# Kernel optimization log

Hardware: AMD Instinct MI355X
Metric: run time of the kernel (lower is better)

## Reference

```python
import jax, jax.numpy as jnp
import numpy as np

D_MODEL = 512
HIDDEN = 2 * D_MODEL
B, L = 8, 2048
R_MIN, R_MAX = 0.8, 0.99
LN_EPS = 1e-5


def setup_inputs() -> dict:
    key = jax.random.key(0)
    ks = jax.random.split(key, 12)
    x = jax.random.normal(ks[0], (B, L, D_MODEL), jnp.float32)
    mask = jnp.ones((B, L), jnp.float32)
    # LRU eigenvalue init, exactly as the torch __init__
    u1 = jax.random.uniform(ks[1], (HIDDEN,), jnp.float32)
    u2 = jax.random.uniform(ks[2], (HIDDEN,), jnp.float32)
    nu_log = jnp.log(-0.5 * jnp.log(u1 * (R_MAX ** 2 - R_MIN ** 2) + R_MIN ** 2))
    theta_log = jnp.log(u2 * 2.0 * np.pi)
    diag_lambda = jnp.exp(jax.lax.complex(-jnp.exp(nu_log), jnp.exp(theta_log)))
    gamma_log = jnp.log(jnp.sqrt(1.0 - jnp.abs(diag_lambda) ** 2))
    params_log = jnp.stack([nu_log, theta_log, gamma_log])  # (3, HIDDEN)
    s_in = 1.0 / np.sqrt(D_MODEL)
    s_out = 1.0 / np.sqrt(HIDDEN)
    # complex Linear weights (real+imag parts; trained weights are fully complex)
    W_in_re = jax.random.uniform(ks[3], (HIDDEN, D_MODEL), jnp.float32, -s_in, s_in)
    W_in_im = jax.random.uniform(ks[4], (HIDDEN, D_MODEL), jnp.float32, -s_in, s_in)
    b_in_re = jax.random.uniform(ks[5], (HIDDEN,), jnp.float32, -s_in, s_in)
    b_in_im = jax.random.uniform(ks[6], (HIDDEN,), jnp.float32, -s_in, s_in)
    W_out_re = jax.random.uniform(ks[7], (D_MODEL, HIDDEN), jnp.float32, -s_out, s_out)
    W_out_im = jax.random.uniform(ks[8], (D_MODEL, HIDDEN), jnp.float32, -s_out, s_out)
    b_out_re = jax.random.uniform(ks[9], (D_MODEL,), jnp.float32, -s_out, s_out)
    b_out_im = jax.random.uniform(ks[10], (D_MODEL,), jnp.float32, -s_out, s_out)
    ln_w = jnp.ones((D_MODEL,), jnp.float32)
    ln_b = jnp.zeros((D_MODEL,), jnp.float32)
    return dict(x=x, mask=mask, params_log=params_log,
                W_in_re=W_in_re, W_in_im=W_in_im, b_in_re=b_in_re, b_in_im=b_in_im,
                W_out_re=W_out_re, W_out_im=W_out_im, b_out_re=b_out_re, b_out_im=b_out_im,
                ln_w=ln_w, ln_b=ln_b)


def _lru_parallel_scan(h, lamb, mask, Bn, Ln, Dn):
    # log-depth doubling trick over complex diagonal recurrence (faithful port)
    log2_L = int(np.ceil(np.log2(Ln)))
    for i in range(1, log2_L + 1):
        l = 2 ** i
        h = h.reshape(Bn * Ln // l, l, Dn)
        m = mask.reshape(Bn * Ln // l, l)
        h1, h2 = h[:, : l // 2], h[:, l // 2 :]
        if i > 1:
            lamb = jnp.concatenate([lamb, lamb * lamb[-1]], axis=0)  # powers lam^1..lam^(l/2)
        h2 = h2 + lamb * h1[:, -1:] * m[:, l // 2 - 1 : l // 2, None]
        h = jnp.concatenate([h1, h2], axis=1)
    return h.reshape(Bn, Ln, Dn)


def reference(x, mask, params_log, W_in_re, W_in_im, b_in_re, b_in_im,
              W_out_re, W_out_im, b_out_re, b_out_im, ln_w, ln_b):
    nu, theta, gamma = jnp.exp(params_log)  # each (HIDDEN,)
    lamb = jnp.exp(jax.lax.complex(-nu, theta))[None, :]  # (1, HIDDEN)
    W_in = jax.lax.complex(W_in_re, W_in_im)
    b_in = jax.lax.complex(b_in_re, b_in_im)
    W_out = jax.lax.complex(W_out_re, W_out_im)
    b_out = jax.lax.complex(b_out_re, b_out_im)
    xc = x.astype(jnp.complex64)
    h = (jnp.einsum('bld,hd->blh', xc, W_in) + b_in) * gamma  # (B, L, HIDDEN) complex64
    Bn, Ln, Dn = h.shape
    h = _lru_parallel_scan(h, lamb, mask, Bn, Ln, Dn)
    y = (jnp.einsum('blh,dh->bld', h, W_out) + b_out).real + x  # dropout = identity (eval)
    mean = jnp.mean(y, axis=-1, keepdims=True)
    var = jnp.var(y, axis=-1, keepdims=True)
    return (y - mean) / jnp.sqrt(var + LN_EPS) * ln_w + ln_b
```

## Files before the change

kernel.cpp:

```cpp
#include <hip/hip_runtime.h>
#include <hip/hip_bf16.h>
#include <cstdint>
#include <cstddef>


typedef unsigned short u16;
typedef __attribute__((ext_vector_type(8))) short bf16x8;
typedef __attribute__((ext_vector_type(4))) float f32x4;

#define B_    8
#define L_    2048
#define D_    512
#define H_    1024
#define M_    (B_ * L_)
#define SEG_  128
#define T_    (L_ / SEG_)

__device__ __forceinline__ float b2f(u16 u) {
  union { unsigned int i; float f; } v; v.i = ((unsigned int)u) << 16; return v.f;
}
__device__ __forceinline__ u16 f2b(float f) {
  union { float f; unsigned int i; } v; v.f = f;
  unsigned int x = v.i;
  return (u16)((x + 0x7fffu + ((x >> 16) & 1u)) >> 16);
}

__device__ __forceinline__ void gl2lds16(const void* g, void* l) {
  __builtin_amdgcn_global_load_lds(
      (const __attribute__((address_space(1))) void*)g,
      (__attribute__((address_space(3))) void*)l, 16, 0, 0);
}

__device__ __forceinline__ int ksw(int row, int kc) {
  return (kc ^ (row & 3) ^ ((row >> 2) & 3)) & 3;
}

__global__ __launch_bounds__(256) void conv_f32_bf16(
    const float* __restrict__ in, u16* __restrict__ out, int n4)
{
  int i = blockIdx.x * 256 + threadIdx.x;
  if (i < n4) {
    float4 v = ((const float4*)in)[i];
    ushort4 o;
    o.x = f2b(v.x); o.y = f2b(v.y); o.z = f2b(v.z); o.w = f2b(v.w);
    ((ushort4*)out)[i] = o;
  }
}

__global__ __launch_bounds__(256) void prep_weights(
    const float* __restrict__ wire, const float* __restrict__ wiim,
    const float* __restrict__ wore, const float* __restrict__ woim,
    const float* __restrict__ bire, const float* __restrict__ biim,
    const float* __restrict__ params,
    u16* __restrict__ winb, u16* __restrict__ wcat, float* __restrict__ bb)
{
  int i = blockIdx.x * 256 + threadIdx.x;
  float g = expf(params[2 * H_ + (i >> 9)]);
  winb[i]           = f2b(wire[i] * g);
  winb[H_ * D_ + i] = f2b(wiim[i] * g);
  int d = i >> 10, c = i & 1023;
  wcat[(size_t)d * 2048 + c]        = f2b(wore[i]);
  wcat[(size_t)d * 2048 + 1024 + c] = f2b(-woim[i]);
  if (i < 2048) {
    float gb = expf(params[2 * H_ + (i & (H_ - 1))]);
    bb[i] = ((i < 1024) ? bire[i] : biim[i - 1024]) * gb;
  }
}

template <int MODE>
__global__ __launch_bounds__(256, 4) void gemm_bt(
    const u16* __restrict__ A, const u16* __restrict__ Bp, int K,
    void* __restrict__ outp, int ldc, const float* __restrict__ p0)
{
  __shared__ __align__(16) u16 sA[128 * 32];
  __shared__ __align__(16) u16 sB[128 * 32];

  const int tid  = threadIdx.x;
  const int lane = tid & 63;
  const int wave = tid >> 6;
  const int wm = wave >> 1, wn = wave & 1;
  const int m0 = blockIdx.x * 128;
  const int n0 = blockIdx.y * 128;

  f32x4 acc[4][4];
#pragma unroll
  for (int i = 0; i < 4; ++i)
#pragma unroll
    for (int j = 0; j < 4; ++j) { f32x4 z = {0.f, 0.f, 0.f, 0.f}; acc[i][j] = z; }

  const int q = lane >> 4;
  const int r = lane & 15;

  for (int k0 = 0; k0 < K; k0 += 32) {
#pragma unroll
    for (int it = 0; it < 2; ++it) {
      int ci  = it * 256 + tid;
      int row = ci >> 2;
      int kc  = ksw(row, ci & 3);
      gl2lds16(A  + (size_t)(m0 + row) * K + k0 + kc * 8, &sA[ci * 8]);
      gl2lds16(Bp + (size_t)(n0 + row) * K + k0 + kc * 8, &sB[ci * 8]);
    }
    __syncthreads();

    bf16x8 af[4], bfv[4];
#pragma unroll
    for (int mt = 0; mt < 4; ++mt) {
      int arow = wm * 64 + mt * 16 + r;
      int slot = (arow << 2) | ksw(arow, q);
      af[mt] = *(const bf16x8*)&sA[slot * 8];
    }
#pragma unroll
    for (int nt = 0; nt < 4; ++nt) {
      int brow = wn * 64 + nt * 16 + r;
      int slot = (brow << 2) | ksw(brow, q);
      bfv[nt] = *(const bf16x8*)&sB[slot * 8];
    }
#pragma unroll
    for (int mt = 0; mt < 4; ++mt)
#pragma unroll
      for (int nt = 0; nt < 4; ++nt)
        acc[mt][nt] = __builtin_amdgcn_mfma_f32_16x16x32_bf16(
            bfv[nt], af[mt], acc[mt][nt], 0, 0, 0);
    __syncthreads();
  }

#pragma unroll
  for (int nt = 0; nt < 4; ++nt) {
    const int nb = n0 + wn * 64 + nt * 16 + q * 4;
    const float4 b4 = *(const float4*)&p0[nb];
#pragma unroll
    for (int mt = 0; mt < 4; ++mt) {
      const int mg = m0 + wm * 64 + mt * 16 + r;
      if (MODE == 0) {
        ushort4 o;
        o.x = f2b(acc[mt][nt][0] + b4.x);
        o.y = f2b(acc[mt][nt][1] + b4.y);
        o.z = f2b(acc[mt][nt][2] + b4.z);
        o.w = f2b(acc[mt][nt][3] + b4.w);
        *(ushort4*)&((u16*)outp)[(size_t)mg * ldc + nb] = o;
      } else {
        float4 o;
        o.x = acc[mt][nt][0] + b4.x;
        o.y = acc[mt][nt][1] + b4.y;
        o.z = acc[mt][nt][2] + b4.z;
        o.w = acc[mt][nt][3] + b4.w;
        *(float4*)&((float*)outp)[(size_t)mg * ldc + nb] = o;
      }
    }
  }
}

__global__ __launch_bounds__(256) void scan_fin(
    const u16* __restrict__ h, const float* __restrict__ mask,
    const float* __restrict__ params, float2* __restrict__ segfin,
    float* __restrict__ prodm)
{
  const int s = blockIdx.x, b = blockIdx.y;
  const int c4 = threadIdx.x * 4;
  float lr[4], li[4];
#pragma unroll
  for (int j = 0; j < 4; ++j) {
    int c = c4 + j;
    float nu = expf(params[c]);
    float th = expf(params[H_ + c]);
    float mg = expf(-nu);
    lr[j] = mg * cosf(th);
    li[j] = mg * sinf(th);
  }
  const int t0 = s * T_;
  const u16* p = h + (size_t)(b * L_ + t0) * (2 * H_) + c4;
  const float* mp = mask + b * L_ + t0;
  float fac0;
  if (t0 == 0) fac0 = 0.f; else fac0 = mask[b * L_ + t0 - 1];

  ushort4 re[T_], im[T_];
#pragma unroll
  for (int j = 0; j < T_; ++j) {
    re[j] = *(const ushort4*)(p + (size_t)j * 2 * H_);
    im[j] = *(const ushort4*)(p + (size_t)j * 2 * H_ + H_);
  }
  float mf[T_];
  mf[0] = fac0;
#pragma unroll
  for (int j = 1; j < T_; ++j) mf[j] = mp[j - 1];

  float sr[4] = {0, 0, 0, 0}, si[4] = {0, 0, 0, 0};
  float pm = 1.f;
#pragma unroll
  for (int i = 0; i < T_; ++i) {
    float fac = mf[i];
    pm *= fac;
    u16 rr[4], ii[4];
    *(ushort4*)rr = re[i]; *(ushort4*)ii = im[i];
#pragma unroll
    for (int k = 0; k < 4; ++k) {
      float ar = fac * sr[k], ai = fac * si[k];
      sr[k] = b2f(rr[k]) + lr[k] * ar - li[k] * ai;
      si[k] = b2f(ii[k]) + lr[k] * ai + li[k] * ar;
    }
  }
#pragma unroll
  for (int j = 0; j < 4; ++j)
    segfin[(size_t)(b * SEG_ + s) * H_ + c4 + j] = make_float2(sr[j], si[j]);
  if (threadIdx.x == 0) prodm[b * SEG_ + s] = pm;
}

__global__ __launch_bounds__(256) void scan_carry(
    const float2* __restrict__ segfin, const float* __restrict__ prodm,
    const float* __restrict__ params, float2* __restrict__ carries)
{
  int idx = blockIdx.x * 256 + threadIdx.x;
  int b = idx >> 10, c = idx & 1023;
  float nu = expf(params[c]);
  float th = expf(params[H_ + c]);
  float mg = expf(-nu);
  float ltr = mg * cosf(th), lti = mg * sinf(th);
#pragma unroll
  for (int sq = 0; sq < 4; ++sq) {
    float nr = ltr * ltr - lti * lti;
    float ni = 2.f * ltr * lti;
    ltr = nr; lti = ni;
  }
  float cr = 0.f, ci = 0.f;
  float2 fin = segfin[(size_t)(b * SEG_) * H_ + c];
  float pmv = prodm[b * SEG_];
  for (int s = 0; s < SEG_; ++s) {
    size_t o = (size_t)(b * SEG_ + s) * H_ + c;
    carries[o] = make_float2(cr, ci);
    float2 finn; float pmn;
    if (s + 1 < SEG_) { finn = segfin[o + H_]; pmn = prodm[b * SEG_ + s + 1]; }
    float nr = fin.x + pmv * (ltr * cr - lti * ci);
    float ni = fin.y + pmv * (ltr * ci + lti * cr);
    cr = nr; ci = ni;
    fin = finn; pmv = pmn;
  }
}

__global__ __launch_bounds__(256) void scan_full(
    u16* __restrict__ h, const float* __restrict__ mask,
    const float* __restrict__ params, const float2* __restrict__ carries)
{
  const int s = blockIdx.x, b = blockIdx.y;
  const int c4 = threadIdx.x * 4;
  float lr[4], li[4], sr[4], si[4];
#pragma unroll
  for (int j = 0; j < 4; ++j) {
    int c = c4 + j;
    float nu = expf(params[c]);
    float th = expf(params[H_ + c]);
    float mg = expf(-nu);
    lr[j] = mg * cosf(th);
    li[j] = mg * sinf(th);
    float2 cv = carries[(size_t)(b * SEG_ + s) * H_ + c];
    sr[j] = cv.x; si[j] = cv.y;
  }
  const int t0 = s * T_;
  u16* p = h + (size_t)(b * L_ + t0) * (2 * H_) + c4;
  const float* mp = mask + b * L_ + t0;
  float fac0;
  if (t0 == 0) fac0 = 0.f; else fac0 = mask[b * L_ + t0 - 1];

  ushort4 re[T_], im[T_];
#pragma unroll
  for (int j = 0; j < T_; ++j) {
    re[j] = *(const ushort4*)(p + (size_t)j * 2 * H_);
    im[j] = *(const ushort4*)(p + (size_t)j * 2 * H_ + H_);
  }
  float mf[T_];
  mf[0] = fac0;
#pragma unroll
  for (int j = 1; j < T_; ++j) mf[j] = mp[j - 1];

#pragma unroll
  for (int i = 0; i < T_; ++i) {
    float fac = mf[i];
    u16 rr[4], ii[4], orr[4], oii[4];
    *(ushort4*)rr = re[i]; *(ushort4*)ii = im[i];
#pragma unroll
    for (int j = 0; j < 4; ++j) {
      float ar = fac * sr[j], ai = fac * si[j];
      float nr2 = b2f(rr[j]) + lr[j] * ar - li[j] * ai;
      float ni2 = b2f(ii[j]) + lr[j] * ai + li[j] * ar;
      sr[j] = nr2; si[j] = ni2;
      orr[j] = f2b(nr2); oii[j] = f2b(ni2);
    }
    *(ushort4*)(p + (size_t)i * 2 * H_)      = *(ushort4*)orr;
    *(ushort4*)(p + (size_t)i * 2 * H_ + H_) = *(ushort4*)oii;
  }
}

__global__ __launch_bounds__(256) void ln_kernel(
    const float* __restrict__ y, const float* __restrict__ xg,
    const float* __restrict__ lnw, const float* __restrict__ lnb,
    float* __restrict__ out)
{
  const int wave = threadIdx.x >> 6, lane = threadIdx.x & 63;
  const size_t row = (size_t)blockIdx.x * 4 + wave;
  const float* yr = y + row * 512;
  const float* xr = xg + row * 512;
  float z[8];
  { float4 t = *(const float4*)&yr[lane * 4];        z[0]=t.x; z[1]=t.y; z[2]=t.z; z[3]=t.w; }
  { float4 t = *(const float4*)&yr[256 + lane * 4];  z[4]=t.x; z[5]=t.y; z[6]=t.z; z[7]=t.w; }
  { float4 t = *(const float4*)&xr[lane * 4];        z[0]+=t.x; z[1]+=t.y; z[2]+=t.z; z[3]+=t.w; }
  { float4 t = *(const float4*)&xr[256 + lane * 4];  z[4]+=t.x; z[5]+=t.y; z[6]+=t.z; z[7]+=t.w; }
  float s = 0.f, ss = 0.f;
#pragma unroll
  for (int j = 0; j < 8; ++j) { s += z[j]; ss += z[j] * z[j]; }
#pragma unroll
  for (int o = 32; o > 0; o >>= 1) { s += __shfl_xor(s, o); ss += __shfl_xor(ss, o); }
  const float mean = s * (1.f / 512.f);
  const float var  = ss * (1.f / 512.f) - mean * mean;
  const float inv  = rsqrtf(var + 1e-5f);
  float ov[8];
#pragma unroll
  for (int j = 0; j < 8; ++j) {
    int col = (j < 4) ? (lane * 4 + j) : (256 + lane * 4 + (j - 4));
    ov[j] = (z[j] - mean) * inv * lnw[col] + lnb[col];
  }
  { float4 t; t.x=ov[0]; t.y=ov[1]; t.z=ov[2]; t.w=ov[3];
    *(float4*)&out[row * 512 + lane * 4] = t; }
  { float4 t; t.x=ov[4]; t.y=ov[5]; t.z=ov[6]; t.w=ov[7];
    *(float4*)&out[row * 512 + 256 + lane * 4] = t; }
}

extern "C" void kernel_launch(void* const* d_in, const int* in_sizes, int n_in,
                              void* d_out, int out_size, void* d_ws, size_t ws_size,
                              hipStream_t stream) {
  (void)in_sizes; (void)n_in; (void)out_size; (void)ws_size;
  const float* x      = (const float*)d_in[0];
  const float* mask   = (const float*)d_in[1];
  const float* params = (const float*)d_in[2];
  const float* Wire   = (const float*)d_in[3];
  const float* Wiim   = (const float*)d_in[4];
  const float* bire   = (const float*)d_in[5];
  const float* biim   = (const float*)d_in[6];
  const float* Wore   = (const float*)d_in[7];
  const float* Woim   = (const float*)d_in[8];
  const float* bore   = (const float*)d_in[9];
  const float* lnw    = (const float*)d_in[11];
  const float* lnb    = (const float*)d_in[12];

  char* ws = (char*)d_ws;
  u16*    xb      = (u16*)   (ws);
  float2* segfin  = (float2*)(ws);
  float2* carries = (float2*)(ws + (size_t)8388608);
  float*  prodm   = (float*) (ws + (size_t)16777216);
  float*  y       = (float*) (ws);
  u16*    h       = (u16*)   (ws + (size_t)33554432);
  u16*    winb    = (u16*)   (ws + (size_t)100663296);
  u16*    wcat    = (u16*)   (ws + (size_t)102760448);
  float*  bb      = (float*) (ws + (size_t)104857600);

  conv_f32_bf16<<<8192, 256, 0, stream>>>(x, xb, M_ * D_ / 4);
  prep_weights<<<2048, 256, 0, stream>>>(Wire, Wiim, Wore, Woim, bire, biim,
                                         params, winb, wcat, bb);

  gemm_bt<0><<<dim3(128, 16), 256, 0, stream>>>(
      xb, winb, 512, (void*)h, 2048, bb);

  scan_fin<<<dim3(SEG_, B_), 256, 0, stream>>>(h, mask, params, segfin, prodm);
  scan_carry<<<32, 256, 0, stream>>>(segfin, prodm, params, carries);
  scan_full<<<dim3(SEG_, B_), 256, 0, stream>>>(h, mask, params, carries);

  gemm_bt<1><<<dim3(128, 4), 256, 0, stream>>>(
      h, wcat, 2048, (void*)y, 512, bore);

  ln_kernel<<<4096, 256, 0, stream>>>(y, x, lnw, lnb, (float*)d_out);
}
```

Baseline: 284.5 us.

## Load GEMM fragments directly from global memory and lengthen scan segments

The GEMMs drop LDS staging and barriers. Each wave now loads its MFMA fragments straight from global memory into registers and prefetches the next k-step into a second register set, with the occupancy hint lowered to 3. The scan halves the segment count, so each segment covers 32 steps, and streams inputs in double-buffered chunks of 8 steps instead of preloading every step. The carry kernel squares lambda one more time to match the new segment length. Loading from global memory removes the sync overhead but gives up LDS sharing, so the same tile data is fetched by several waves and more global/L2 traffic is likely.

```diff
diff --git a/kernel.cpp b/kernel.cpp
--- a/kernel.cpp
+++ b/kernel.cpp
@@ -13,7 +13,7 @@
 #define D_    512
 #define H_    1024
 #define M_    (B_ * L_)
-#define SEG_  128
+#define SEG_  64
 #define T_    (L_ / SEG_)
 
 __device__ __forceinline__ float b2f(u16 u) {
@@ -23,16 +23,6 @@
   union { float f; unsigned int i; } v; v.f = f;
   unsigned int x = v.i;
   return (u16)((x + 0x7fffu + ((x >> 16) & 1u)) >> 16);
-}
-
-__device__ __forceinline__ void gl2lds16(const void* g, void* l) {
-  __builtin_amdgcn_global_load_lds(
-      (const __attribute__((address_space(1))) void*)g,
-      (__attribute__((address_space(3))) void*)l, 16, 0, 0);
-}
-
-__device__ __forceinline__ int ksw(int row, int kc) {
-  return (kc ^ (row & 3) ^ ((row >> 2) & 3)) & 3;
 }
 
 __global__ __launch_bounds__(256) void conv_f32_bf16(
@@ -68,13 +58,10 @@
 }
 
 template <int MODE>
-__global__ __launch_bounds__(256, 4) void gemm_bt(
+__global__ __launch_bounds__(256, 3) void gemm_direct(
     const u16* __restrict__ A, const u16* __restrict__ Bp, int K,
     void* __restrict__ outp, int ldc, const float* __restrict__ p0)
 {
-  __shared__ __align__(16) u16 sA[128 * 32];
-  __shared__ __align__(16) u16 sB[128 * 32];
-
   const int tid  = threadIdx.x;
   const int lane = tid & 63;
   const int wave = tid >> 6;
@@ -82,52 +69,49 @@
   const int m0 = blockIdx.x * 128;
   const int n0 = blockIdx.y * 128;
 
-  f32x4 acc[4][4];
-#pragma unroll
-  for (int i = 0; i < 4; ++i)
-#pragma unroll
-    for (int j = 0; j < 4; ++j) { f32x4 z = {0.f, 0.f, 0.f, 0.f}; acc[i][j] = z; }
-
   const int q = lane >> 4;
   const int r = lane & 15;
 
+  const u16* aptr = A  + (size_t)(m0 + wm * 64 + r) * K + q * 8;
+  const u16* bptr = Bp + (size_t)(n0 + wn * 64 + r) * K + q * 8;
+  const size_t strideA = (size_t)16 * K;
+
+  f32x4 acc[4][4];
+#pragma unroll
+  for (int i = 0; i < 4; ++i)
+#pragma unroll
+    for (int j = 0; j < 4; ++j) { f32x4 z = {0.f, 0.f, 0.f, 0.f}; acc[i][j] = z; }
+
+  bf16x8 ca[4], cb[4], na[4], nb[4];
+#pragma unroll
+  for (int t = 0; t < 4; ++t) {
+    ca[t] = *(const bf16x8*)(aptr + t * strideA);
+    cb[t] = *(const bf16x8*)(bptr + t * strideA);
+  }
+
+#pragma unroll 2
   for (int k0 = 0; k0 < K; k0 += 32) {
-#pragma unroll
-    for (int it = 0; it < 2; ++it) {
-      int ci  = it * 256 + tid;
-      int row = ci >> 2;
-      int kc  = ksw(row, ci & 3);
-      gl2lds16(A  + (size_t)(m0 + row) * K + k0 + kc * 8, &sA[ci * 8]);
-      gl2lds16(Bp + (size_t)(n0 + row) * K + k0 + kc * 8, &sB[ci * 8]);
-    }
-    __syncthreads();
-
-    bf16x8 af[4], bfv[4];
-#pragma unroll
-    for (int mt = 0; mt < 4; ++mt) {
-      int arow = wm * 64 + mt * 16 + r;
-      int slot = (arow << 2) | ksw(arow, q);
-      af[mt] = *(const bf16x8*)&sA[slot * 8];
-    }
-#pragma unroll
-    for (int nt = 0; nt < 4; ++nt) {
-      int brow = wn * 64 + nt * 16 + r;
-      int slot = (brow << 2) | ksw(brow, q);
-      bfv[nt] = *(const bf16x8*)&sB[slot * 8];
+    if (k0 + 32 < K) {
+#pragma unroll
+      for (int t = 0; t < 4; ++t) {
+        na[t] = *(const bf16x8*)(aptr + t * strideA + k0 + 32);
+        nb[t] = *(const bf16x8*)(bptr + t * strideA + k0 + 32);
+      }
     }
 #pragma unroll
     for (int mt = 0; mt < 4; ++mt)
 #pragma unroll
       for (int nt = 0; nt < 4; ++nt)
         acc[mt][nt] = __builtin_amdgcn_mfma_f32_16x16x32_bf16(
-            bfv[nt], af[mt], acc[mt][nt], 0, 0, 0);
-    __syncthreads();
+            cb[nt], ca[mt], acc[mt][nt], 0, 0, 0);
+#pragma unroll
+    for (int t = 0; t < 4; ++t) { ca[t] = na[t]; cb[t] = nb[t]; }
   }
 
 #pragma unroll
   for (int nt = 0; nt < 4; ++nt) {
-    const int nb = n0 + wn * 64 + nt * 16 + q * 4;
-    const float4 b4 = *(const float4*)&p0[nb];
+    const int nb4 = n0 + wn * 64 + nt * 16 + q * 4;
+    const float4 b4 = *(const float4*)&p0[nb4];
 #pragma unroll
     for (int mt = 0; mt < 4; ++mt) {
       const int mg = m0 + wm * 64 + mt * 16 + r;
@@ -137,14 +121,14 @@
         o.y = f2b(acc[mt][nt][1] + b4.y);
         o.z = f2b(acc[mt][nt][2] + b4.z);
         o.w = f2b(acc[mt][nt][3] + b4.w);
-        *(ushort4*)&((u16*)outp)[(size_t)mg * ldc + nb] = o;
+        *(ushort4*)&((u16*)outp)[(size_t)mg * ldc + nb4] = o;
       } else {
         float4 o;
         o.x = acc[mt][nt][0] + b4.x;
         o.y = acc[mt][nt][1] + b4.y;
         o.z = acc[mt][nt][2] + b4.z;
         o.w = acc[mt][nt][3] + b4.w;
-        *(float4*)&((float*)outp)[(size_t)mg * ldc + nb] = o;
+        *(float4*)&((float*)outp)[(size_t)mg * ldc + nb4] = o;
       }
     }
   }
@@ -173,30 +157,38 @@
   float fac0;
   if (t0 == 0) fac0 = 0.f; else fac0 = mask[b * L_ + t0 - 1];
 
-  ushort4 re[T_], im[T_];
-#pragma unroll
-  for (int j = 0; j < T_; ++j) {
-    re[j] = *(const ushort4*)(p + (size_t)j * 2 * H_);
-    im[j] = *(const ushort4*)(p + (size_t)j * 2 * H_ + H_);
-  }
-  float mf[T_];
-  mf[0] = fac0;
-#pragma unroll
-  for (int j = 1; j < T_; ++j) mf[j] = mp[j - 1];
-
+  ushort4 bre[2][8], bim[2][8];
+#pragma unroll
+  for (int j = 0; j < 8; ++j) {
+    bre[0][j] = *(const ushort4*)(p + (size_t)j * 2 * H_);
+    bim[0][j] = *(const ushort4*)(p + (size_t)j * 2 * H_ + H_);
+  }
   float sr[4] = {0, 0, 0, 0}, si[4] = {0, 0, 0, 0};
   float pm = 1.f;
 #pragma unroll
-  for (int i = 0; i < T_; ++i) {
-    float fac = mf[i];
-    pm *= fac;
-    u16 rr[4], ii[4];
-    *(ushort4*)rr = re[i]; *(ushort4*)ii = im[i];
-#pragma unroll
-    for (int k = 0; k < 4; ++k) {
-      float ar = fac * sr[k], ai = fac * si[k];
-      sr[k] = b2f(rr[k]) + lr[k] * ar - li[k] * ai;
-      si[k] = b2f(ii[k]) + lr[k] * ai + li[k] * ar;
+  for (int ch = 0; ch < T_ / 8; ++ch) {
+    const int cur = ch & 1, nxt = cur ^ 1;
+    if (ch < T_ / 8 - 1) {
+      const u16* pn = p + (size_t)(ch + 1) * 8 * 2 * H_;
+#pragma unroll
+      for (int j = 0; j < 8; ++j) {
+        bre[nxt][j] = *(const ushort4*)(pn + (size_t)j * 2 * H_);
+        bim[nxt][j] = *(const ushort4*)(pn + (size_t)j * 2 * H_ + H_);
+      }
+    }
+#pragma unroll
+    for (int j = 0; j < 8; ++j) {
+      int i = ch * 8 + j;
+      float fac = (i == 0) ? fac0 : mp[i - 1];
+      pm *= fac;
+      u16 rr[4], ii[4];
+      *(ushort4*)rr = bre[cur][j]; *(ushort4*)ii = bim[cur][j];
+#pragma unroll
+      for (int k = 0; k < 4; ++k) {
+        float ar = fac * sr[k], ai = fac * si[k];
+        sr[k] = b2f(rr[k]) + lr[k] * ar - li[k] * ai;
+        si[k] = b2f(ii[k]) + lr[k] * ai + li[k] * ar;
+      }
     }
   }
 #pragma unroll
@@ -216,7 +208,7 @@
   float mg = expf(-nu);
   float ltr = mg * cosf(th), lti = mg * sinf(th);
 #pragma unroll
-  for (int sq = 0; sq < 4; ++sq) {
+  for (int sq = 0; sq < 5; ++sq) {
     float nr = ltr * ltr - lti * lti;
     float ni = 2.f * ltr * lti;
     ltr = nr; lti = ni;
@@ -260,32 +252,40 @@
   float fac0;
   if (t0 == 0) fac0 = 0.f; else fac0 = mask[b * L_ + t0 - 1];
 
-  ushort4 re[T_], im[T_];
-#pragma unroll
-  for (int j = 0; j < T_; ++j) {
-    re[j] = *(const ushort4*)(p + (size_t)j * 2 * H_);
-    im[j] = *(const ushort4*)(p + (size_t)j * 2 * H_ + H_);
-  }
-  float mf[T_];
-  mf[0] = fac0;
-#pragma unroll
-  for (int j = 1; j < T_; ++j) mf[j] = mp[j - 1];
-
-#pragma unroll
-  for (int i = 0; i < T_; ++i) {
-    float fac = mf[i];
-    u16 rr[4], ii[4], orr[4], oii[4];
-    *(ushort4*)rr = re[i]; *(ushort4*)ii = im[i];
-#pragma unroll
-    for (int j = 0; j < 4; ++j) {
-      float ar = fac * sr[j], ai = fac * si[j];
-      float nr2 = b2f(rr[j]) + lr[j] * ar - li[j] * ai;
-      float ni2 = b2f(ii[j]) + lr[j] * ai + li[j] * ar;
-      sr[j] = nr2; si[j] = ni2;
-      orr[j] = f2b(nr2); oii[j] = f2b(ni2);
-    }
-    *(ushort4*)(p + (size_t)i * 2 * H_)      = *(ushort4*)orr;
-    *(ushort4*)(p + (size_t)i * 2 * H_ + H_) = *(ushort4*)oii;
+  ushort4 bre[2][8], bim[2][8];
+#pragma unroll
+  for (int j = 0; j < 8; ++j) {
+    bre[0][j] = *(const ushort4*)(p + (size_t)j * 2 * H_);
+    bim[0][j] = *(const ushort4*)(p + (size_t)j * 2 * H_ + H_);
+  }
+#pragma unroll
+  for (int ch = 0; ch < T_ / 8; ++ch) {
+    const int cur = ch & 1, nxt = cur ^ 1;
+    if (ch < T_ / 8 - 1) {
+      const u16* pn = p + (size_t)(ch + 1) * 8 * 2 * H_;
+#pragma unroll
+      for (int j = 0; j < 8; ++j) {
+        bre[nxt][j] = *(const ushort4*)(pn + (size_t)j * 2 * H_);
+        bim[nxt][j] = *(const ushort4*)(pn + (size_t)j * 2 * H_ + H_);
+      }
+    }
+#pragma unroll
+    for (int j = 0; j < 8; ++j) {
+      int i = ch * 8 + j;
+      float fac = (i == 0) ? fac0 : mp[i - 1];
+      u16 rr[4], ii[4], orr[4], oii[4];
+      *(ushort4*)rr = bre[cur][j]; *(ushort4*)ii = bim[cur][j];
+#pragma unroll
+      for (int k = 0; k < 4; ++k) {
+        float ar = fac * sr[k], ai = fac * si[k];
+        float nr2 = b2f(rr[k]) + lr[k] * ar - li[k] * ai;
+        float ni2 = b2f(ii[k]) + lr[k] * ai + li[k] * ar;
+        sr[k] = nr2; si[k] = ni2;
+        orr[k] = f2b(nr2); oii[k] = f2b(ni2);
+      }
+      *(ushort4*)(p + (size_t)i * 2 * H_)      = *(ushort4*)orr;
+      *(ushort4*)(p + (size_t)i * 2 * H_ + H_) = *(ushort4*)oii;
+    }
   }
 }
 
@@ -343,8 +343,8 @@
   char* ws = (char*)d_ws;
   u16*    xb      = (u16*)   (ws);
   float2* segfin  = (float2*)(ws);
-  float2* carries = (float2*)(ws + (size_t)8388608);
-  float*  prodm   = (float*) (ws + (size_t)16777216);
+  float2* carries = (float2*)(ws + (size_t)4194304);
+  float*  prodm   = (float*) (ws + (size_t)8388608);
   float*  y       = (float*) (ws);
   u16*    h       = (u16*)   (ws + (size_t)33554432);
   u16*    winb    = (u16*)   (ws + (size_t)100663296);
@@ -355,14 +355,14 @@
   prep_weights<<<2048, 256, 0, stream>>>(Wire, Wiim, Wore, Woim, bire, biim,
                                          params, winb, wcat, bb);
 
-  gemm_bt<0><<<dim3(128, 16), 256, 0, stream>>>(
+  gemm_direct<0><<<dim3(128, 16), 256, 0, stream>>>(
       xb, winb, 512, (void*)h, 2048, bb);
 
   scan_fin<<<dim3(SEG_, B_), 256, 0, stream>>>(h, mask, params, segfin, prodm);
   scan_carry<<<32, 256, 0, stream>>>(segfin, prodm, params, carries);
   scan_full<<<dim3(SEG_, B_), 256, 0, stream>>>(h, mask, params, carries);
 
-  gemm_bt<1><<<dim3(128, 4), 256, 0, stream>>>(
+  gemm_direct<1><<<dim3(128, 4), 256, 0, stream>>>(
       h, wcat, 2048, (void*)y, 512, bore);
 
   ln_kernel<<<4096, 256, 0, stream>>>(y, x, lnw, lnb, (float*)d_out);
```

After: 409.4 us. +43.9%, slower.
